# Kernel optimization log

Measured on AMD Instinct MI355X. Metric: run time of the kernel, lower is better.

The kernel has to match this reference:

```python
import jax, jax.numpy as jnp
import numpy as np

H = 16  # num_heads
NEG = -1e9


def setup_inputs() -> dict:
    key = jax.random.key(0)
    ks = jax.random.split(key, 12)
    T, B, E, M = 2048, 2, 1024, 1024
    s = E ** -0.5
    inp = {
        "query": jax.random.normal(ks[0], (T, B, E), jnp.float32),
        "position_encoding": jax.random.normal(ks[1], (H, T, T), jnp.float32) * 0.02,
        "long_context_retrieval": jax.random.normal(ks[2], (2, M, B, E), jnp.float32),
        "q_w": jax.random.normal(ks[3], (E, E), jnp.float32) * s,
        "q_b": jnp.zeros((E,), jnp.float32),
        "k_w": jax.random.normal(ks[4], (E, E), jnp.float32) * s,
        "k_b": jnp.zeros((E,), jnp.float32),
        "v_w": jax.random.normal(ks[5], (E, E), jnp.float32) * s,
        "v_b": jnp.zeros((E,), jnp.float32),
        "out_w": jax.random.normal(ks[6], (E, E), jnp.float32) * s,
        "out_b": jnp.zeros((E,), jnp.float32),
        "memory_bias": jnp.zeros((H,), jnp.float32),
    }
    return inp


def reference(query, position_encoding, long_context_retrieval,
              q_w, q_b, k_w, k_b, v_w, v_b, out_w, out_b, memory_bias):
    T, B, E = query.shape
    D = E // H
    scaling = D ** -0.5

    def proj(x, w, b):
        # x: [L, B, E] -> [B, H, L, D]
        L = x.shape[0]
        y = jnp.einsum('lbe,fe->lbf', x, w) + b
        return y.reshape(L, B, H, D).transpose(1, 2, 0, 3)

    q = proj(query, q_w, q_b) * scaling          # [B,H,T,D]
    k = proj(query, k_w, k_b)                    # [B,H,T,D]
    v = proj(query, v_w, v_b)                    # [B,H,T,D]

    # local attention with per-head position encoding and causal mask
    scores = jnp.einsum('bhtd,bhsd->bhts', q, k) + position_encoding[None]
    causal = jnp.triu(jnp.ones((T, T), bool), k=1)
    scores = jnp.where(causal[None, None], NEG, scores)
    attn_local = jax.nn.softmax(scores, axis=-1)
    out_local = jnp.einsum('bhts,bhsd->bhtd', attn_local, v)

    # attention over retrieved long-context memory (keys/values projected)
    km = proj(long_context_retrieval[0], k_w, k_b)   # [B,H,M,D]
    vm = proj(long_context_retrieval[1], v_w, v_b)   # [B,H,M,D]
    mem_scores = jnp.einsum('bhtd,bhmd->bhtm', q, km)
    attn_mem = jax.nn.softmax(mem_scores, axis=-1)
    out_mem = jnp.einsum('bhtm,bhmd->bhtd', attn_mem, vm)

    # per-head learned gate: weighted sum of local and memory outputs
    g = jax.nn.sigmoid(memory_bias)[None, :, None, None]
    out = (1.0 - g) * out_local + g * out_mem        # [B,H,T,D]

    out = out.transpose(2, 0, 1, 3).reshape(T, B, E)
    return jnp.einsum('tbe,fe->tbf', out, out_w) + out_b
```

## Files before the change

### kernel.cpp

```cpp
#include <hip/hip_runtime.h>

typedef __bf16 bf16_t;
typedef __bf16 bf16x8 __attribute__((ext_vector_type(8)));
typedef float floatx4 __attribute__((ext_vector_type(4)));

#define MFMA16(a, b, c) __builtin_amdgcn_mfma_f32_16x16x32_bf16((a), (b), (c), 0, 0, 0)

__global__ void detect_kernel(const unsigned short* __restrict__ q, int* flag)
{
    __shared__ int cnt;
    if (threadIdx.x == 0) cnt = 0;
    __syncthreads();
    int local = 0;
    for (int i = threadIdx.x; i < 65536; i += 256) {
        unsigned short u = q[i];
        if ((u & 0x7F80u) == 0x7F80u) local++;
    }
    atomicAdd(&cnt, local);
    __syncthreads();
    if (threadIdx.x == 0) flag[0] = (cnt >= 8) ? 1 : 0;
}

__device__ inline void cvt16_f32(const float* __restrict__ p, bf16x8& lo, bf16x8& hi)
{
    float4 a = ((const float4*)p)[0];
    float4 b = ((const float4*)p)[1];
    float4 c = ((const float4*)p)[2];
    float4 d = ((const float4*)p)[3];
    lo[0] = (bf16_t)a.x; lo[1] = (bf16_t)a.y; lo[2] = (bf16_t)a.z; lo[3] = (bf16_t)a.w;
    lo[4] = (bf16_t)b.x; lo[5] = (bf16_t)b.y; lo[6] = (bf16_t)b.z; lo[7] = (bf16_t)b.w;
    hi[0] = (bf16_t)c.x; hi[1] = (bf16_t)c.y; hi[2] = (bf16_t)c.z; hi[3] = (bf16_t)c.w;
    hi[4] = (bf16_t)d.x; hi[5] = (bf16_t)d.y; hi[6] = (bf16_t)d.z; hi[7] = (bf16_t)d.w;
}

__global__ __launch_bounds__(256) void gemm_bt_kernel(
    const void* __restrict__ Xv, const void* __restrict__ Wv,
    const void* __restrict__ biasv, void* __restrict__ Yv,
    const int* __restrict__ flag,
    int K, int N, float scale, int mode, int Brows, int Tdim, int xext,
    size_t xelemoff)
{
    __shared__ __attribute__((aligned(16))) bf16_t As[128 * 40];
    __shared__ __attribute__((aligned(16))) bf16_t Bs[128 * 40];

    const int f32 = flag[0];
    const int xf32 = xext ? f32 : 0;

    const int tid = threadIdx.x;
    const int wv = tid >> 6, lane = tid & 63;
    const int qd = lane >> 4, l16 = lane & 15;
    const int wm = (wv >> 1) * 64, wn = (wv & 1) * 64;
    const int rm0 = blockIdx.x * 128, cn0 = blockIdx.y * 128;

    const int srow = tid >> 1;
    const int sseg = (tid & 1) * 16;
    const size_t xoff = xelemoff + (size_t)(rm0 + srow) * K + sseg;
    const size_t woff = (size_t)(cn0 + srow) * K + sseg;
    const bf16_t* Xh = (const bf16_t*)Xv + xoff;
    const float*  Xf = (const float*)Xv + xoff;
    const bf16_t* Wh = (const bf16_t*)Wv + woff;
    const float*  Wf = (const float*)Wv + woff;
    bf16_t* Asw = &As[srow * 40 + sseg];
    bf16_t* Bsw = &Bs[srow * 40 + sseg];

    floatx4 acc[4][4];
#pragma unroll
    for (int i = 0; i < 4; i++)
#pragma unroll
        for (int j = 0; j < 4; j++) acc[i][j] = (floatx4){0.f, 0.f, 0.f, 0.f};

    for (int k0 = 0; k0 < K; k0 += 32) {
        bf16x8 x0, x1, w0, w1;
        if (xf32) {
            cvt16_f32(Xf + k0, x0, x1);
        } else {
            x0 = *(const bf16x8*)(Xh + k0);
            x1 = *(const bf16x8*)(Xh + k0 + 8);
        }
        if (f32) {
            cvt16_f32(Wf + k0, w0, w1);
        } else {
            w0 = *(const bf16x8*)(Wh + k0);
            w1 = *(const bf16x8*)(Wh + k0 + 8);
        }
        __syncthreads();
        *(bf16x8*)(Asw) = x0;
        *(bf16x8*)(Asw + 8) = x1;
        *(bf16x8*)(Bsw) = w0;
        *(bf16x8*)(Bsw + 8) = w1;
        __syncthreads();

        bf16x8 af[4], bfg[4];
#pragma unroll
        for (int mi = 0; mi < 4; mi++)
            af[mi] = *(const bf16x8*)(&As[(wm + mi * 16 + l16) * 40 + qd * 8]);
#pragma unroll
        for (int ni = 0; ni < 4; ni++)
            bfg[ni] = *(const bf16x8*)(&Bs[(wn + ni * 16 + l16) * 40 + qd * 8]);
#pragma unroll
        for (int mi = 0; mi < 4; mi++)
#pragma unroll
            for (int ni = 0; ni < 4; ni++)
                acc[mi][ni] = MFMA16(af[mi], bfg[ni], acc[mi][ni]);
    }

#pragma unroll
    for (int ni = 0; ni < 4; ni++) {
        const int col = cn0 + wn + ni * 16 + l16;
        const float bv = f32 ? ((const float*)biasv)[col]
                             : (float)((const bf16_t*)biasv)[col];
#pragma unroll
        for (int mi = 0; mi < 4; mi++) {
            const int row0 = rm0 + wm + mi * 16 + qd * 4;
#pragma unroll
            for (int r = 0; r < 4; r++) {
                const int row = row0 + r;
                const float val = (acc[mi][ni][r] + bv) * scale;
                if (mode == 0) {
                    if (f32) ((float*)Yv)[(size_t)row * N + col] = val;
                    else ((bf16_t*)Yv)[(size_t)row * N + col] = (bf16_t)val;
                } else {
                    const int t = row / Brows, b = row % Brows;
                    const int h = col >> 6, d = col & 63;
                    ((bf16_t*)Yv)[(((size_t)(b * 16 + h) * Tdim) + t) * 64 + d] = (bf16_t)val;
                }
            }
        }
    }
}

__global__ __launch_bounds__(256) void attn_kernel(
    const bf16_t* __restrict__ Qg, const bf16_t* __restrict__ Kg,
    const bf16_t* __restrict__ Vg, const bf16_t* __restrict__ KMg,
    const bf16_t* __restrict__ VMg, const void* __restrict__ posv,
    const void* __restrict__ mbiasv, bf16_t* __restrict__ att,
    const int* __restrict__ flag, int T, int Mlen)
{
    __shared__ __attribute__((aligned(16))) bf16_t Qs[64 * 72];
    __shared__ __attribute__((aligned(16))) bf16_t Ks[64 * 72];
    __shared__ __attribute__((aligned(16))) bf16_t Vts[64 * 72];
    __shared__ __attribute__((aligned(16))) bf16_t Ps[4][16 * 72];

    const int f32 = flag[0];
    const int tid = threadIdx.x;
    const int wv = tid >> 6, lane = tid & 63;
    const int qd = lane >> 4, l16 = lane & 15;
    const int qt = blockIdx.x;
    const int bh = blockIdx.y;
    const int h = bh & 15;
    const int t0 = qt * 64;

    const bf16_t* Qb = Qg + (size_t)bh * T * 64;
    const bf16_t* Kb = Kg + (size_t)bh * T * 64;
    const bf16_t* Vb = Vg + (size_t)bh * T * 64;
    const bf16_t* KMb = KMg + (size_t)bh * Mlen * 64;
    const bf16_t* VMb = VMg + (size_t)bh * Mlen * 64;
    const float*  posf = (const float*)posv + (size_t)h * T * T;
    const bf16_t* posh = (const bf16_t*)posv + (size_t)h * T * T;

    const int srow = tid >> 2;
    const int sseg = (tid & 3) * 16;

    {
        bf16x8 v0 = *(const bf16x8*)(Qb + (size_t)(t0 + srow) * 64 + sseg);
        bf16x8 v1 = *(const bf16x8*)(Qb + (size_t)(t0 + srow) * 64 + sseg + 8);
        *(bf16x8*)(&Qs[srow * 72 + sseg]) = v0;
        *(bf16x8*)(&Qs[srow * 72 + sseg + 8]) = v1;
    }
    __syncthreads();
    const bf16x8 a0 = *(const bf16x8*)(&Qs[(wv * 16 + l16) * 72 + qd * 8]);
    const bf16x8 a1 = *(const bf16x8*)(&Qs[(wv * 16 + l16) * 72 + 32 + qd * 8]);

    floatx4 Ol[4], Om[4];
    float ml[4], ll[4], mm2[4], lm[4];
#pragma unroll
    for (int i = 0; i < 4; i++) {
        Ol[i] = (floatx4){0.f, 0.f, 0.f, 0.f};
        Om[i] = (floatx4){0.f, 0.f, 0.f, 0.f};
        ml[i] = -1e9f; ll[i] = 0.f; mm2[i] = -1e9f; lm[i] = 0.f;
    }

    const int trow_base = t0 + wv * 16 + qd * 4;
    bf16_t* Pw = &Ps[wv][0];

    for (int st = 0; st <= qt; ++st) {
        const int s0 = st * 64;
        __syncthreads();
        {
            const bf16_t* Kp = Kb + (size_t)(s0 + srow) * 64 + sseg;
            bf16x8 kv0 = *(const bf16x8*)(Kp);
            bf16x8 kv1 = *(const bf16x8*)(Kp + 8);
            *(bf16x8*)(&Ks[srow * 72 + sseg]) = kv0;
            *(bf16x8*)(&Ks[srow * 72 + sseg + 8]) = kv1;
            const bf16_t* Vp = Vb + (size_t)(s0 + srow) * 64 + sseg;
            bf16x8 vv0 = *(const bf16x8*)(Vp);
            bf16x8 vv1 = *(const bf16x8*)(Vp + 8);
#pragma unroll
            for (int j = 0; j < 8; j++) Vts[(sseg + j) * 72 + srow] = vv0[j];
#pragma unroll
            for (int j = 0; j < 8; j++) Vts[(sseg + 8 + j) * 72 + srow] = vv1[j];
        }
        __syncthreads();

        float sv[4][4];
        const bool diag = (st == qt);
#pragma unroll
        for (int ni = 0; ni < 4; ni++) {
            floatx4 c = (floatx4){0.f, 0.f, 0.f, 0.f};
            bf16x8 b0 = *(const bf16x8*)(&Ks[(ni * 16 + l16) * 72 + qd * 8]);
            bf16x8 b1 = *(const bf16x8*)(&Ks[(ni * 16 + l16) * 72 + 32 + qd * 8]);
            c = MFMA16(a0, b0, c);
            c = MFMA16(a1, b1, c);
            const int sg = s0 + ni * 16 + l16;
#pragma unroll
            for (int r = 0; r < 4; r++) {
                const int tg = trow_base + r;
                const size_t pidx = (size_t)tg * T + sg;
                const float pe = f32 ? posf[pidx] : (float)posh[pidx];
                float val = c[r] + pe;
                if (diag && sg > tg) val = -1e9f;
                sv[ni][r] = val;
            }
        }

#pragma unroll
        for (int r = 0; r < 4; r++) {
            float mt = fmaxf(fmaxf(sv[0][r], sv[1][r]), fmaxf(sv[2][r], sv[3][r]));
            mt = fmaxf(mt, __shfl_xor(mt, 1));
            mt = fmaxf(mt, __shfl_xor(mt, 2));
            mt = fmaxf(mt, __shfl_xor(mt, 4));
            mt = fmaxf(mt, __shfl_xor(mt, 8));
            const float mnew = fmaxf(ml[r], mt);
            const float alpha = __expf(ml[r] - mnew);
            ml[r] = mnew;
            float ls = 0.f;
#pragma unroll
            for (int ni = 0; ni < 4; ni++) {
                const float p = __expf(sv[ni][r] - mnew);
                sv[ni][r] = p;
                ls += p;
            }
            ls += __shfl_xor(ls, 1);
            ls += __shfl_xor(ls, 2);
            ls += __shfl_xor(ls, 4);
            ls += __shfl_xor(ls, 8);
            ll[r] = ll[r] * alpha + ls;
#pragma unroll
            for (int ni = 0; ni < 4; ni++) Ol[ni][r] *= alpha;
#pragma unroll
            for (int ni = 0; ni < 4; ni++)
                Pw[(qd * 4 + r) * 72 + ni * 16 + l16] = (bf16_t)sv[ni][r];
        }
        __syncthreads();
#pragma unroll
        for (int ks = 0; ks < 2; ks++) {
            bf16x8 pf = *(const bf16x8*)(&Pw[l16 * 72 + ks * 32 + qd * 8]);
#pragma unroll
            for (int ni = 0; ni < 4; ni++) {
                bf16x8 vf = *(const bf16x8*)(&Vts[(ni * 16 + l16) * 72 + ks * 32 + qd * 8]);
                Ol[ni] = MFMA16(pf, vf, Ol[ni]);
            }
        }
    }

    for (int st = 0; st < Mlen / 64; ++st) {
        const int s0 = st * 64;
        __syncthreads();
        {
            const bf16_t* Kp = KMb + (size_t)(s0 + srow) * 64 + sseg;
            bf16x8 kv0 = *(const bf16x8*)(Kp);
            bf16x8 kv1 = *(const bf16x8*)(Kp + 8);
            *(bf16x8*)(&Ks[srow * 72 + sseg]) = kv0;
            *(bf16x8*)(&Ks[srow * 72 + sseg + 8]) = kv1;
            const bf16_t* Vp = VMb + (size_t)(s0 + srow) * 64 + sseg;
            bf16x8 vv0 = *(const bf16x8*)(Vp);
            bf16x8 vv1 = *(const bf16x8*)(Vp + 8);
#pragma unroll
            for (int j = 0; j < 8; j++) Vts[(sseg + j) * 72 + srow] = vv0[j];
#pragma unroll
            for (int j = 0; j < 8; j++) Vts[(sseg + 8 + j) * 72 + srow] = vv1[j];
        }
        __syncthreads();

        float sv[4][4];
#pragma unroll
        for (int ni = 0; ni < 4; ni++) {
            floatx4 c = (floatx4){0.f, 0.f, 0.f, 0.f};
            bf16x8 b0 = *(const bf16x8*)(&Ks[(ni * 16 + l16) * 72 + qd * 8]);
            bf16x8 b1 = *(const bf16x8*)(&Ks[(ni * 16 + l16) * 72 + 32 + qd * 8]);
            c = MFMA16(a0, b0, c);
            c = MFMA16(a1, b1, c);
#pragma unroll
            for (int r = 0; r < 4; r++) sv[ni][r] = c[r];
        }

#pragma unroll
        for (int r = 0; r < 4; r++) {
            float mt = fmaxf(fmaxf(sv[0][r], sv[1][r]), fmaxf(sv[2][r], sv[3][r]));
            mt = fmaxf(mt, __shfl_xor(mt, 1));
            mt = fmaxf(mt, __shfl_xor(mt, 2));
            mt = fmaxf(mt, __shfl_xor(mt, 4));
            mt = fmaxf(mt, __shfl_xor(mt, 8));
            const float mnew = fmaxf(mm2[r], mt);
            const float alpha = __expf(mm2[r] - mnew);
            mm2[r] = mnew;
            float ls = 0.f;
#pragma unroll
            for (int ni = 0; ni < 4; ni++) {
                const float p = __expf(sv[ni][r] - mnew);
                sv[ni][r] = p;
                ls += p;
            }
            ls += __shfl_xor(ls, 1);
            ls += __shfl_xor(ls, 2);
            ls += __shfl_xor(ls, 4);
            ls += __shfl_xor(ls, 8);
            lm[r] = lm[r] * alpha + ls;
#pragma unroll
            for (int ni = 0; ni < 4; ni++) Om[ni][r] *= alpha;
#pragma unroll
            for (int ni = 0; ni < 4; ni++)
                Pw[(qd * 4 + r) * 72 + ni * 16 + l16] = (bf16_t)sv[ni][r];
        }
        __syncthreads();
#pragma unroll
        for (int ks = 0; ks < 2; ks++) {
            bf16x8 pf = *(const bf16x8*)(&Pw[l16 * 72 + ks * 32 + qd * 8]);
#pragma unroll
            for (int ni = 0; ni < 4; ni++) {
                bf16x8 vf = *(const bf16x8*)(&Vts[(ni * 16 + l16) * 72 + ks * 32 + qd * 8]);
                Om[ni] = MFMA16(pf, vf, Om[ni]);
            }
        }
    }

    const float gb = f32 ? ((const float*)mbiasv)[h] : (float)((const bf16_t*)mbiasv)[h];
    const float g = 1.f / (1.f + __expf(-gb));
    const int b = bh >> 4;
#pragma unroll
    for (int ni = 0; ni < 4; ni++) {
        const int col = h * 64 + ni * 16 + l16;
#pragma unroll
        for (int r = 0; r < 4; r++) {
            const int tg = trow_base + r;
            const float ol = Ol[ni][r] / ll[r];
            const float om = Om[ni][r] / lm[r];
            const float val = (1.f - g) * ol + g * om;
            att[(size_t)(tg * 2 + b) * 1024 + col] = (bf16_t)val;
        }
    }
}

__global__ void sentinel_kernel(float* o) { o[0] = 30000.0f; }

extern "C" void kernel_launch(void* const* d_in, const int* in_sizes, int n_in,
                              void* d_out, int out_size, void* d_ws, size_t ws_size,
                              hipStream_t stream)
{
    const void* query = d_in[0];
    const void* pos   = d_in[1];
    const void* lcr   = d_in[2];
    const void* q_w   = d_in[3];
    const void* q_b   = d_in[4];
    const void* k_w   = d_in[5];
    const void* k_b   = d_in[6];
    const void* v_w   = d_in[7];
    const void* v_b   = d_in[8];
    const void* out_w = d_in[9];
    const void* out_b = d_in[10];
    const void* mbias = d_in[11];

    const int T = 2048, B = 2, E = 1024, M = 1024;

    const size_t elems = (size_t)(3 * B * 16 * T * 64 + 2 * B * 16 * M * 64 + T * B * E);
    const size_t needed = elems * 2 + 64;
    if (ws_size < needed) {
        sentinel_kernel<<<1, 1, 0, stream>>>((float*)d_out);
        return;
    }

    bf16_t* q_ws  = (bf16_t*)d_ws;
    bf16_t* k_ws  = q_ws + (size_t)B * 16 * T * 64;
    bf16_t* v_ws  = k_ws + (size_t)B * 16 * T * 64;
    bf16_t* km_ws = v_ws + (size_t)B * 16 * T * 64;
    bf16_t* vm_ws = km_ws + (size_t)B * 16 * M * 64;
    bf16_t* att_ws = vm_ws + (size_t)B * 16 * M * 64;
    int* flag = (int*)((char*)d_ws + elems * 2);

    dim3 blk(256);
    dim3 g1(T * B / 128, E / 128);
    dim3 g2(M * B / 128, E / 128);
    dim3 ga(T / 64, B * 16);

    const float scaling = 0.125f;
    const size_t lcr_half = (size_t)M * B * E;

    detect_kernel<<<1, 256, 0, stream>>>((const unsigned short*)query, flag);
    gemm_bt_kernel<<<g1, blk, 0, stream>>>(query, q_w, q_b, q_ws, flag, E, E, scaling, 1, B, T, 1, 0);
    gemm_bt_kernel<<<g1, blk, 0, stream>>>(query, k_w, k_b, k_ws, flag, E, E, 1.0f, 1, B, T, 1, 0);
    gemm_bt_kernel<<<g1, blk, 0, stream>>>(query, v_w, v_b, v_ws, flag, E, E, 1.0f, 1, B, T, 1, 0);
    gemm_bt_kernel<<<g2, blk, 0, stream>>>(lcr, k_w, k_b, km_ws, flag, E, E, 1.0f, 1, B, M, 1, 0);
    gemm_bt_kernel<<<g2, blk, 0, stream>>>(lcr, v_w, v_b, vm_ws, flag, E, E, 1.0f, 1, B, M, 1, lcr_half);
    attn_kernel<<<ga, blk, 0, stream>>>(q_ws, k_ws, v_ws, km_ws, vm_ws, pos, mbias, att_ws, flag, T, M);
    gemm_bt_kernel<<<g1, blk, 0, stream>>>(att_ws, out_w, out_b, d_out, flag, E, E, 1.0f, 0, B, T, 0, 0);
    (void)in_sizes; (void)n_in; (void)out_size;
}
```

Baseline: 982.1 us.

## Fuse projections into one launch, pre-transpose V, drop LDS staging in attention

Merges the five projection GEMMs into a single grid-partitioned kernel. V and memory-V are written pre-transposed so the attention kernel can load K and V^T fragments straight from global memory, with no LDS staging or block-wide barriers. Masked diagonal tiles skip their QK MFMAs. The output projection uses a new 64-row GEMM tile to get more blocks. The risk is more uncoalesced global traffic, since K/V reuse across waves now depends on cache instead of shared memory, plus scattered 2-element stores of the transposed V.

```diff
diff --git a/kernel.cpp b/kernel.cpp
--- a/kernel.cpp
+++ b/kernel.cpp
@@ -1,6 +1,7 @@
 #include <hip/hip_runtime.h>
 
 typedef __bf16 bf16_t;
+typedef __bf16 bf16x2 __attribute__((ext_vector_type(2)));
 typedef __bf16 bf16x8 __attribute__((ext_vector_type(8)));
 typedef float floatx4 __attribute__((ext_vector_type(4)));
 
@@ -33,29 +34,56 @@
     hi[4] = (bf16_t)d.x; hi[5] = (bf16_t)d.y; hi[6] = (bf16_t)d.z; hi[7] = (bf16_t)d.w;
 }
 
-__global__ __launch_bounds__(256) void gemm_bt_kernel(
-    const void* __restrict__ Xv, const void* __restrict__ Wv,
-    const void* __restrict__ biasv, void* __restrict__ Yv,
-    const int* __restrict__ flag,
-    int K, int N, float scale, int mode, int Brows, int Tdim, int xext,
-    size_t xelemoff)
+__global__ __launch_bounds__(256) void proj_kernel(
+    const void* __restrict__ query, const void* __restrict__ lcr,
+    const void* __restrict__ qw, const void* __restrict__ kw,
+    const void* __restrict__ vw,
+    const void* __restrict__ qbias, const void* __restrict__ kbias,
+    const void* __restrict__ vbias,
+    bf16_t* __restrict__ q_ws, bf16_t* __restrict__ k_ws,
+    bf16_t* __restrict__ vt_ws, bf16_t* __restrict__ km_ws,
+    bf16_t* __restrict__ vmt_ws, const int* __restrict__ flag)
 {
     __shared__ __attribute__((aligned(16))) bf16_t As[128 * 40];
     __shared__ __attribute__((aligned(16))) bf16_t Bs[128 * 40];
 
     const int f32 = flag[0];
-    const int xf32 = xext ? f32 : 0;
+    const int K = 1024;
+    const int blk = blockIdx.x;
+
+    int rm0, wcol, mode, Tdim;
+    float scale;
+    const void* Xv; size_t xoff0; const void* Wv; const void* biasv; bf16_t* Yv;
+    if (blk < 768) {
+        rm0 = (blk & 31) * 128;
+        const int cn0 = (blk >> 5) * 128;
+        const int sel = cn0 >> 10;
+        wcol = cn0 & 1023;
+        Xv = query; xoff0 = 0; Tdim = 2048;
+        if (sel == 0)      { Wv = qw; biasv = qbias; Yv = q_ws;  mode = 1; scale = 0.125f; }
+        else if (sel == 1) { Wv = kw; biasv = kbias; Yv = k_ws;  mode = 1; scale = 1.f; }
+        else               { Wv = vw; biasv = vbias; Yv = vt_ws; mode = 2; scale = 1.f; }
+    } else if (blk < 896) {
+        const int b2 = blk - 768;
+        rm0 = (b2 & 15) * 128; wcol = (b2 >> 4) * 128;
+        Xv = lcr; xoff0 = 0;
+        Wv = kw; biasv = kbias; Yv = km_ws; mode = 1; scale = 1.f; Tdim = 1024;
+    } else {
+        const int b2 = blk - 896;
+        rm0 = (b2 & 15) * 128; wcol = (b2 >> 4) * 128;
+        Xv = lcr; xoff0 = (size_t)1024 * 2 * 1024;
+        Wv = vw; biasv = vbias; Yv = vmt_ws; mode = 2; scale = 1.f; Tdim = 1024;
+    }
 
     const int tid = threadIdx.x;
-    const int wv = tid >> 6, lane = tid & 63;
+    const int wvid = tid >> 6, lane = tid & 63;
     const int qd = lane >> 4, l16 = lane & 15;
-    const int wm = (wv >> 1) * 64, wn = (wv & 1) * 64;
-    const int rm0 = blockIdx.x * 128, cn0 = blockIdx.y * 128;
+    const int wm = (wvid >> 1) * 64, wn = (wvid & 1) * 64;
 
     const int srow = tid >> 1;
     const int sseg = (tid & 1) * 16;
-    const size_t xoff = xelemoff + (size_t)(rm0 + srow) * K + sseg;
-    const size_t woff = (size_t)(cn0 + srow) * K + sseg;
+    const size_t xoff = xoff0 + (size_t)(rm0 + srow) * K + sseg;
+    const size_t woff = (size_t)(wcol + srow) * K + sseg;
     const bf16_t* Xh = (const bf16_t*)Xv + xoff;
     const float*  Xf = (const float*)Xv + xoff;
     const bf16_t* Wh = (const bf16_t*)Wv + woff;
@@ -71,15 +99,12 @@
 
     for (int k0 = 0; k0 < K; k0 += 32) {
         bf16x8 x0, x1, w0, w1;
-        if (xf32) {
+        if (f32) {
             cvt16_f32(Xf + k0, x0, x1);
+            cvt16_f32(Wf + k0, w0, w1);
         } else {
             x0 = *(const bf16x8*)(Xh + k0);
             x1 = *(const bf16x8*)(Xh + k0 + 8);
-        }
-        if (f32) {
-            cvt16_f32(Wf + k0, w0, w1);
-        } else {
             w0 = *(const bf16x8*)(Wh + k0);
             w1 = *(const bf16x8*)(Wh + k0 + 8);
         }
@@ -106,70 +131,64 @@
 
 #pragma unroll
     for (int ni = 0; ni < 4; ni++) {
-        const int col = cn0 + wn + ni * 16 + l16;
+        const int col = wcol + wn + ni * 16 + l16;
         const float bv = f32 ? ((const float*)biasv)[col]
                              : (float)((const bf16_t*)biasv)[col];
+        const int hh = col >> 6, dd = col & 63;
 #pragma unroll
         for (int mi = 0; mi < 4; mi++) {
             const int row0 = rm0 + wm + mi * 16 + qd * 4;
-#pragma unroll
-            for (int r = 0; r < 4; r++) {
-                const int row = row0 + r;
-                const float val = (acc[mi][ni][r] + bv) * scale;
-                if (mode == 0) {
-                    if (f32) ((float*)Yv)[(size_t)row * N + col] = val;
-                    else ((bf16_t*)Yv)[(size_t)row * N + col] = (bf16_t)val;
-                } else {
-                    const int t = row / Brows, b = row % Brows;
-                    const int h = col >> 6, d = col & 63;
-                    ((bf16_t*)Yv)[(((size_t)(b * 16 + h) * Tdim) + t) * 64 + d] = (bf16_t)val;
-                }
+            const int t = row0 >> 1;
+            const float v0 = (acc[mi][ni][0] + bv) * scale;
+            const float v1 = (acc[mi][ni][1] + bv) * scale;
+            const float v2 = (acc[mi][ni][2] + bv) * scale;
+            const float v3 = (acc[mi][ni][3] + bv) * scale;
+            if (mode == 1) {
+                Yv[(((size_t)hh * Tdim) + t) * 64 + dd]            = (bf16_t)v0;
+                Yv[(((size_t)(16 + hh) * Tdim) + t) * 64 + dd]     = (bf16_t)v1;
+                Yv[(((size_t)hh * Tdim) + t + 1) * 64 + dd]        = (bf16_t)v2;
+                Yv[(((size_t)(16 + hh) * Tdim) + t + 1) * 64 + dd] = (bf16_t)v3;
+            } else {
+                bf16x2 p0; p0[0] = (bf16_t)v0; p0[1] = (bf16_t)v2;
+                bf16x2 p1; p1[0] = (bf16_t)v1; p1[1] = (bf16_t)v3;
+                *(bf16x2*)&Yv[((size_t)hh * 64 + dd) * Tdim + t] = p0;
+                *(bf16x2*)&Yv[((size_t)(16 + hh) * 64 + dd) * Tdim + t] = p1;
             }
         }
     }
 }
 
+#define PSTR 88
 __global__ __launch_bounds__(256) void attn_kernel(
     const bf16_t* __restrict__ Qg, const bf16_t* __restrict__ Kg,
-    const bf16_t* __restrict__ Vg, const bf16_t* __restrict__ KMg,
-    const bf16_t* __restrict__ VMg, const void* __restrict__ posv,
+    const bf16_t* __restrict__ VTg, const bf16_t* __restrict__ KMg,
+    const bf16_t* __restrict__ VMTg, const void* __restrict__ posv,
     const void* __restrict__ mbiasv, bf16_t* __restrict__ att,
     const int* __restrict__ flag, int T, int Mlen)
 {
-    __shared__ __attribute__((aligned(16))) bf16_t Qs[64 * 72];
-    __shared__ __attribute__((aligned(16))) bf16_t Ks[64 * 72];
-    __shared__ __attribute__((aligned(16))) bf16_t Vts[64 * 72];
-    __shared__ __attribute__((aligned(16))) bf16_t Ps[4][16 * 72];
+    __shared__ __attribute__((aligned(16))) bf16_t Ps[4][16 * PSTR];
 
     const int f32 = flag[0];
     const int tid = threadIdx.x;
     const int wv = tid >> 6, lane = tid & 63;
     const int qd = lane >> 4, l16 = lane & 15;
     const int qt = blockIdx.x;
-    const int bh = blockIdx.y;
-    const int h = bh & 15;
+    const int y = blockIdx.y;
+    const int b = y & 1, h = y >> 1;
+    const int bh = b * 16 + h;
     const int t0 = qt * 64;
-
-    const bf16_t* Qb = Qg + (size_t)bh * T * 64;
-    const bf16_t* Kb = Kg + (size_t)bh * T * 64;
-    const bf16_t* Vb = Vg + (size_t)bh * T * 64;
+    const int tw = t0 + wv * 16;
+
+    const bf16_t* Qb  = Qg  + (size_t)bh * T * 64;
+    const bf16_t* Kb  = Kg  + (size_t)bh * T * 64;
+    const bf16_t* VTb = VTg + (size_t)bh * 64 * T;
     const bf16_t* KMb = KMg + (size_t)bh * Mlen * 64;
-    const bf16_t* VMb = VMg + (size_t)bh * Mlen * 64;
+    const bf16_t* VMTb = VMTg + (size_t)bh * 64 * Mlen;
     const float*  posf = (const float*)posv + (size_t)h * T * T;
     const bf16_t* posh = (const bf16_t*)posv + (size_t)h * T * T;
 
-    const int srow = tid >> 2;
-    const int sseg = (tid & 3) * 16;
-
-    {
-        bf16x8 v0 = *(const bf16x8*)(Qb + (size_t)(t0 + srow) * 64 + sseg);
-        bf16x8 v1 = *(const bf16x8*)(Qb + (size_t)(t0 + srow) * 64 + sseg + 8);
-        *(bf16x8*)(&Qs[srow * 72 + sseg]) = v0;
-        *(bf16x8*)(&Qs[srow * 72 + sseg + 8]) = v1;
-    }
-    __syncthreads();
-    const bf16x8 a0 = *(const bf16x8*)(&Qs[(wv * 16 + l16) * 72 + qd * 8]);
-    const bf16x8 a1 = *(const bf16x8*)(&Qs[(wv * 16 + l16) * 72 + 32 + qd * 8]);
+    const bf16x8 a0 = *(const bf16x8*)(Qb + (size_t)(tw + l16) * 64 + qd * 8);
+    const bf16x8 a1 = *(const bf16x8*)(Qb + (size_t)(tw + l16) * 64 + 32 + qd * 8);
 
     floatx4 Ol[4], Om[4];
     float ml[4], ll[4], mm2[4], lm[4];
@@ -180,46 +199,38 @@
         ml[i] = -1e9f; ll[i] = 0.f; mm2[i] = -1e9f; lm[i] = 0.f;
     }
 
-    const int trow_base = t0 + wv * 16 + qd * 4;
+    const int trow_base = tw + qd * 4;
     bf16_t* Pw = &Ps[wv][0];
 
     for (int st = 0; st <= qt; ++st) {
         const int s0 = st * 64;
-        __syncthreads();
-        {
-            const bf16_t* Kp = Kb + (size_t)(s0 + srow) * 64 + sseg;
-            bf16x8 kv0 = *(const bf16x8*)(Kp);
-            bf16x8 kv1 = *(const bf16x8*)(Kp + 8);
-            *(bf16x8*)(&Ks[srow * 72 + sseg]) = kv0;
-            *(bf16x8*)(&Ks[srow * 72 + sseg + 8]) = kv1;
-            const bf16_t* Vp = Vb + (size_t)(s0 + srow) * 64 + sseg;
-            bf16x8 vv0 = *(const bf16x8*)(Vp);
-            bf16x8 vv1 = *(const bf16x8*)(Vp + 8);
-#pragma unroll
-            for (int j = 0; j < 8; j++) Vts[(sseg + j) * 72 + srow] = vv0[j];
-#pragma unroll
-            for (int j = 0; j < 8; j++) Vts[(sseg + 8 + j) * 72 + srow] = vv1[j];
-        }
-        __syncthreads();
+        const bool diag = (st == qt);
+        const int nhi = diag ? (wv + 1) : 4;
 
         float sv[4][4];
-        const bool diag = (st == qt);
+#pragma unroll
+        for (int ni = 0; ni < 4; ni++)
+#pragma unroll
+            for (int r = 0; r < 4; r++) sv[ni][r] = -1e9f;
+
 #pragma unroll
         for (int ni = 0; ni < 4; ni++) {
-            floatx4 c = (floatx4){0.f, 0.f, 0.f, 0.f};
-            bf16x8 b0 = *(const bf16x8*)(&Ks[(ni * 16 + l16) * 72 + qd * 8]);
-            bf16x8 b1 = *(const bf16x8*)(&Ks[(ni * 16 + l16) * 72 + 32 + qd * 8]);
-            c = MFMA16(a0, b0, c);
-            c = MFMA16(a1, b1, c);
-            const int sg = s0 + ni * 16 + l16;
-#pragma unroll
-            for (int r = 0; r < 4; r++) {
-                const int tg = trow_base + r;
-                const size_t pidx = (size_t)tg * T + sg;
-                const float pe = f32 ? posf[pidx] : (float)posh[pidx];
-                float val = c[r] + pe;
-                if (diag && sg > tg) val = -1e9f;
-                sv[ni][r] = val;
+            if (ni < nhi) {
+                const bf16x8 kb0 = *(const bf16x8*)(Kb + (size_t)(s0 + ni * 16 + l16) * 64 + qd * 8);
+                const bf16x8 kb1 = *(const bf16x8*)(Kb + (size_t)(s0 + ni * 16 + l16) * 64 + 32 + qd * 8);
+                floatx4 c = (floatx4){0.f, 0.f, 0.f, 0.f};
+                c = MFMA16(a0, kb0, c);
+                c = MFMA16(a1, kb1, c);
+                const int sg = s0 + ni * 16 + l16;
+#pragma unroll
+                for (int r = 0; r < 4; r++) {
+                    const int tg = trow_base + r;
+                    const size_t pidx = (size_t)tg * T + sg;
+                    const float pe = f32 ? posf[pidx] : (float)posh[pidx];
+                    float val = c[r] + pe;
+                    if (diag && sg > tg) val = -1e9f;
+                    sv[ni][r] = val;
+                }
             }
         }
 
@@ -249,47 +260,30 @@
             for (int ni = 0; ni < 4; ni++) Ol[ni][r] *= alpha;
 #pragma unroll
             for (int ni = 0; ni < 4; ni++)
-                Pw[(qd * 4 + r) * 72 + ni * 16 + l16] = (bf16_t)sv[ni][r];
-        }
-        __syncthreads();
-#pragma unroll
-        for (int ks = 0; ks < 2; ks++) {
-            bf16x8 pf = *(const bf16x8*)(&Pw[l16 * 72 + ks * 32 + qd * 8]);
-#pragma unroll
-            for (int ni = 0; ni < 4; ni++) {
-                bf16x8 vf = *(const bf16x8*)(&Vts[(ni * 16 + l16) * 72 + ks * 32 + qd * 8]);
-                Ol[ni] = MFMA16(pf, vf, Ol[ni]);
-            }
+                Pw[(qd * 4 + r) * PSTR + ni * 16 + l16] = (bf16_t)sv[ni][r];
+        }
+        asm volatile("s_waitcnt lgkmcnt(0)" ::: "memory");
+        const bf16x8 pf0 = *(const bf16x8*)(&Pw[l16 * PSTR + qd * 8]);
+        const bf16x8 pf1 = *(const bf16x8*)(&Pw[l16 * PSTR + 32 + qd * 8]);
+#pragma unroll
+        for (int ni = 0; ni < 4; ni++) {
+            const bf16x8 vf0 = *(const bf16x8*)(VTb + (size_t)(ni * 16 + l16) * T + s0 + qd * 8);
+            const bf16x8 vf1 = *(const bf16x8*)(VTb + (size_t)(ni * 16 + l16) * T + s0 + 32 + qd * 8);
+            Ol[ni] = MFMA16(pf0, vf0, Ol[ni]);
+            Ol[ni] = MFMA16(pf1, vf1, Ol[ni]);
         }
     }
 
     for (int st = 0; st < Mlen / 64; ++st) {
         const int s0 = st * 64;
-        __syncthreads();
-        {
-            const bf16_t* Kp = KMb + (size_t)(s0 + srow) * 64 + sseg;
-            bf16x8 kv0 = *(const bf16x8*)(Kp);
-            bf16x8 kv1 = *(const bf16x8*)(Kp + 8);
-            *(bf16x8*)(&Ks[srow * 72 + sseg]) = kv0;
-            *(bf16x8*)(&Ks[srow * 72 + sseg + 8]) = kv1;
-            const bf16_t* Vp = VMb + (size_t)(s0 + srow) * 64 + sseg;
-            bf16x8 vv0 = *(const bf16x8*)(Vp);
-            bf16x8 vv1 = *(const bf16x8*)(Vp + 8);
-#pragma unroll
-            for (int j = 0; j < 8; j++) Vts[(sseg + j) * 72 + srow] = vv0[j];
-#pragma unroll
-            for (int j = 0; j < 8; j++) Vts[(sseg + 8 + j) * 72 + srow] = vv1[j];
-        }
-        __syncthreads();
-
         float sv[4][4];
 #pragma unroll
         for (int ni = 0; ni < 4; ni++) {
+            const bf16x8 kb0 = *(const bf16x8*)(KMb + (size_t)(s0 + ni * 16 + l16) * 64 + qd * 8);
+            const bf16x8 kb1 = *(const bf16x8*)(KMb + (size_t)(s0 + ni * 16 + l16) * 64 + 32 + qd * 8);
             floatx4 c = (floatx4){0.f, 0.f, 0.f, 0.f};
-            bf16x8 b0 = *(const bf16x8*)(&Ks[(ni * 16 + l16) * 72 + qd * 8]);
-            bf16x8 b1 = *(const bf16x8*)(&Ks[(ni * 16 + l16) * 72 + 32 + qd * 8]);
-            c = MFMA16(a0, b0, c);
-            c = MFMA16(a1, b1, c);
+            c = MFMA16(a0, kb0, c);
+            c = MFMA16(a1, kb1, c);
 #pragma unroll
             for (int r = 0; r < 4; r++) sv[ni][r] = c[r];
         }
@@ -320,23 +314,22 @@
             for (int ni = 0; ni < 4; ni++) Om[ni][r] *= alpha;
 #pragma unroll
             for (int ni = 0; ni < 4; ni++)
-                Pw[(qd * 4 + r) * 72 + ni * 16 + l16] = (bf16_t)sv[ni][r];
-        }
-        __syncthreads();
-#pragma unroll
-        for (int ks = 0; ks < 2; ks++) {
-            bf16x8 pf = *(const bf16x8*)(&Pw[l16 * 72 + ks * 32 + qd * 8]);
-#pragma unroll
-            for (int ni = 0; ni < 4; ni++) {
-                bf16x8 vf = *(const bf16x8*)(&Vts[(ni * 16 + l16) * 72 + ks * 32 + qd * 8]);
-                Om[ni] = MFMA16(pf, vf, Om[ni]);
-            }
+                Pw[(qd * 4 + r) * PSTR + ni * 16 + l16] = (bf16_t)sv[ni][r];
+        }
+        asm volatile("s_waitcnt lgkmcnt(0)" ::: "memory");
+        const bf16x8 pf0 = *(const bf16x8*)(&Pw[l16 * PSTR + qd * 8]);
+        const bf16x8 pf1 = *(const bf16x8*)(&Pw[l16 * PSTR + 32 + qd * 8]);
+#pragma unroll
+        for (int ni = 0; ni < 4; ni++) {
+            const bf16x8 vf0 = *(const bf16x8*)(VMTb + (size_t)(ni * 16 + l16) * Mlen + s0 + qd * 8);
+            const bf16x8 vf1 = *(const bf16x8*)(VMTb + (size_t)(ni * 16 + l16) * Mlen + s0 + 32 + qd * 8);
+            Om[ni] = MFMA16(pf0, vf0, Om[ni]);
+            Om[ni] = MFMA16(pf1, vf1, Om[ni]);
         }
     }
 
     const float gb = f32 ? ((const float*)mbiasv)[h] : (float)((const bf16_t*)mbiasv)[h];
     const float g = 1.f / (1.f + __expf(-gb));
-    const int b = bh >> 4;
 #pragma unroll
     for (int ni = 0; ni < 4; ni++) {
         const int col = h * 64 + ni * 16 + l16;
@@ -347,6 +340,88 @@
             const float om = Om[ni][r] / lm[r];
             const float val = (1.f - g) * ol + g * om;
             att[(size_t)(tg * 2 + b) * 1024 + col] = (bf16_t)val;
+        }
+    }
+}
+
+__global__ __launch_bounds__(256) void gemm64_kernel(
+    const bf16_t* __restrict__ X, const void* __restrict__ Wv,
+    const void* __restrict__ biasv, void* __restrict__ Yv,
+    const int* __restrict__ flag)
+{
+    __shared__ __attribute__((aligned(16))) bf16_t As[64 * 40];
+    __shared__ __attribute__((aligned(16))) bf16_t Bs[128 * 40];
+
+    const int f32 = flag[0];
+    const int K = 1024, N = 1024;
+    const int tid = threadIdx.x;
+    const int wvid = tid >> 6, lane = tid & 63;
+    const int qd = lane >> 4, l16 = lane & 15;
+    const int wn = wvid * 32;
+    const int rm0 = blockIdx.x * 64, cn0 = blockIdx.y * 128;
+
+    const int arow = tid >> 1;
+    const int aseg = (tid & 1) * 16;
+    const bf16_t* Xp = X + (size_t)(rm0 + (arow & 63)) * K + aseg;
+    const size_t woff = (size_t)(cn0 + arow) * K + aseg;
+    const bf16_t* Wh = (const bf16_t*)Wv + woff;
+    const float*  Wf = (const float*)Wv + woff;
+
+    floatx4 acc[4][2];
+#pragma unroll
+    for (int i = 0; i < 4; i++)
+#pragma unroll
+        for (int j = 0; j < 2; j++) acc[i][j] = (floatx4){0.f, 0.f, 0.f, 0.f};
+
+    for (int k0 = 0; k0 < K; k0 += 32) {
+        bf16x8 x0, x1, w0, w1;
+        if (tid < 128) {
+            x0 = *(const bf16x8*)(Xp + k0);
+            x1 = *(const bf16x8*)(Xp + k0 + 8);
+        }
+        if (f32) cvt16_f32(Wf + k0, w0, w1);
+        else {
+            w0 = *(const bf16x8*)(Wh + k0);
+            w1 = *(const bf16x8*)(Wh + k0 + 8);
+        }
+        __syncthreads();
+        if (tid < 128) {
+            *(bf16x8*)&As[arow * 40 + aseg] = x0;
+            *(bf16x8*)&As[arow * 40 + aseg + 8] = x1;
+        }
+        *(bf16x8*)&Bs[arow * 40 + aseg] = w0;
+        *(bf16x8*)&Bs[arow * 40 + aseg + 8] = w1;
+        __syncthreads();
+
+        bf16x8 af[4], bfg[2];
+#pragma unroll
+        for (int mi = 0; mi < 4; mi++)
+            af[mi] = *(const bf16x8*)(&As[(mi * 16 + l16) * 40 + qd * 8]);
+#pragma unroll
+        for (int ni = 0; ni < 2; ni++)
+            bfg[ni] = *(const bf16x8*)(&Bs[(wn + ni * 16 + l16) * 40 + qd * 8]);
+#pragma unroll
+        for (int mi = 0; mi < 4; mi++)
+#pragma unroll
+            for (int ni = 0; ni < 2; ni++)
+                acc[mi][ni] = MFMA16(af[mi], bfg[ni], acc[mi][ni]);
+    }
+
+#pragma unroll
+    for (int ni = 0; ni < 2; ni++) {
+        const int col = cn0 + wn + ni * 16 + l16;
+        const float bv = f32 ? ((const float*)biasv)[col]
+                             : (float)((const bf16_t*)biasv)[col];
+#pragma unroll
+        for (int mi = 0; mi < 4; mi++) {
+            const int row0 = rm0 + mi * 16 + qd * 4;
+#pragma unroll
+            for (int r = 0; r < 4; r++) {
+                const int row = row0 + r;
+                const float val = acc[mi][ni][r] + bv;
+                if (f32) ((float*)Yv)[(size_t)row * N + col] = val;
+                else ((bf16_t*)Yv)[(size_t)row * N + col] = (bf16_t)val;
+            }
         }
     }
 }
@@ -379,29 +454,21 @@
         return;
     }
 
-    bf16_t* q_ws  = (bf16_t*)d_ws;
-    bf16_t* k_ws  = q_ws + (size_t)B * 16 * T * 64;
-    bf16_t* v_ws  = k_ws + (size_t)B * 16 * T * 64;
-    bf16_t* km_ws = v_ws + (size_t)B * 16 * T * 64;
-    bf16_t* vm_ws = km_ws + (size_t)B * 16 * M * 64;
-    bf16_t* att_ws = vm_ws + (size_t)B * 16 * M * 64;
+    bf16_t* q_ws   = (bf16_t*)d_ws;
+    bf16_t* k_ws   = q_ws + (size_t)B * 16 * T * 64;
+    bf16_t* vt_ws  = k_ws + (size_t)B * 16 * T * 64;
+    bf16_t* km_ws  = vt_ws + (size_t)B * 16 * T * 64;
+    bf16_t* vmt_ws = km_ws + (size_t)B * 16 * M * 64;
+    bf16_t* att_ws = vmt_ws + (size_t)B * 16 * M * 64;
     int* flag = (int*)((char*)d_ws + elems * 2);
 
-    dim3 blk(256);
-    dim3 g1(T * B / 128, E / 128);
-    dim3 g2(M * B / 128, E / 128);
-    dim3 ga(T / 64, B * 16);
-
-    const float scaling = 0.125f;
-    const size_t lcr_half = (size_t)M * B * E;
-
     detect_kernel<<<1, 256, 0, stream>>>((const unsigned short*)query, flag);
-    gemm_bt_kernel<<<g1, blk, 0, stream>>>(query, q_w, q_b, q_ws, flag, E, E, scaling, 1, B, T, 1, 0);
-    gemm_bt_kernel<<<g1, blk, 0, stream>>>(query, k_w, k_b, k_ws, flag, E, E, 1.0f, 1, B, T, 1, 0);
-    gemm_bt_kernel<<<g1, blk, 0, stream>>>(query, v_w, v_b, v_ws, flag, E, E, 1.0f, 1, B, T, 1, 0);
-    gemm_bt_kernel<<<g2, blk, 0, stream>>>(lcr, k_w, k_b, km_ws, flag, E, E, 1.0f, 1, B, M, 1, 0);
-    gemm_bt_kernel<<<g2, blk, 0, stream>>>(lcr, v_w, v_b, vm_ws, flag, E, E, 1.0f, 1, B, M, 1, lcr_half);
-    attn_kernel<<<ga, blk, 0, stream>>>(q_ws, k_ws, v_ws, km_ws, vm_ws, pos, mbias, att_ws, flag, T, M);
-    gemm_bt_kernel<<<g1, blk, 0, stream>>>(att_ws, out_w, out_b, d_out, flag, E, E, 1.0f, 0, B, T, 0, 0);
+    proj_kernel<<<1024, 256, 0, stream>>>(query, lcr, q_w, k_w, v_w,
+                                          q_b, k_b, v_b,
+                                          q_ws, k_ws, vt_ws, km_ws, vmt_ws, flag);
+    attn_kernel<<<dim3(T / 64, 32), 256, 0, stream>>>(
+        q_ws, k_ws, vt_ws, km_ws, vmt_ws, pos, mbias, att_ws, flag, T, M);
+    gemm64_kernel<<<dim3(T * B / 64, E / 128), 256, 0, stream>>>(
+        att_ws, out_w, out_b, d_out, flag);
     (void)in_sizes; (void)n_in; (void)out_size;
 }
```

Measured after the change: 888.3 us. -9.6%, faster.
